# Performance work log

Hardware: AMD Instinct MI355X
Metric: run time of the kernel (lower is better)

## Reference

```python
import jax, jax.numpy as jnp
import numpy as np

HIDDEN = 2048
NUM_HEADS = 16
HEAD_DIM = HIDDEN // NUM_HEADS
WORLD_SIZE = 4
BATCH = 1
SEQ_SHARD = 2048


def setup_inputs() -> dict:
    key = jax.random.key(0)
    ks = jax.random.split(key, 9)
    s = 1.0 / np.sqrt(HIDDEN)
    return {
        'hidden_states': jax.random.normal(ks[0], (BATCH, SEQ_SHARD, HIDDEN), jnp.float32),
        'wq': jax.random.normal(ks[1], (HIDDEN, HIDDEN), jnp.float32) * s,
        'bq': jax.random.normal(ks[2], (HIDDEN,), jnp.float32) * s,
        'wk': jax.random.normal(ks[3], (HIDDEN, HIDDEN), jnp.float32) * s,
        'bk': jax.random.normal(ks[4], (HIDDEN,), jnp.float32) * s,
        'wv': jax.random.normal(ks[5], (HIDDEN, HIDDEN), jnp.float32) * s,
        'bv': jax.random.normal(ks[6], (HIDDEN,), jnp.float32) * s,
        'wo': jax.random.normal(ks[7], (HIDDEN, HIDDEN), jnp.float32) * s,
        'bo': jax.random.normal(ks[8], (HIDDEN,), jnp.float32) * s,
    }


def _ring_attention(q, k, v):
    # q, k, v: [B, H, S, D]. Simulation: every ring step receives the SAME
    # local KV shard (all_k_shards are clones of k), accumulated with
    # flash-style online softmax across WORLD_SIZE steps.
    B, H, S, D = q.shape
    scale = 1.0 / np.sqrt(D)
    output_acc = jnp.zeros_like(q)
    max_score = jnp.full((B, H, S, 1), -jnp.inf, dtype=q.dtype)
    sum_exp = jnp.zeros((B, H, S, 1), dtype=q.dtype)
    for _ in range(WORLD_SIZE):  # fixed small loop over ring steps
        scores = jnp.einsum('bhsd,bhtd->bhst', q, k) * scale  # [B,H,S,S]
        new_max = jnp.max(scores, axis=-1, keepdims=True)
        combined_max = jnp.maximum(max_score, new_max)
        old_scale = jnp.exp(max_score - combined_max)
        new_scale = jnp.exp(new_max - combined_max)
        new_exp = jnp.exp(scores - new_max)
        sum_exp = sum_exp * old_scale + jnp.sum(new_exp, axis=-1, keepdims=True) * new_scale
        output_acc = output_acc * old_scale + jnp.einsum('bhst,bhtd->bhsd', new_exp, v) * new_scale
        max_score = combined_max
    return output_acc / sum_exp


def reference(hidden_states, wq, bq, wk, bk, wv, bv, wo, bo):
    B, S, _ = hidden_states.shape
    # nn.Linear: y = x @ W^T + b
    q = hidden_states @ wq.T + bq
    k = hidden_states @ wk.T + bk
    v = hidden_states @ wv.T + bv
    split = lambda t: t.reshape(B, S, NUM_HEADS, HEAD_DIM).transpose(0, 2, 1, 3)
    attn = _ring_attention(split(q), split(k), split(v))  # [B,H,S,D]
    attn = attn.transpose(0, 2, 1, 3).reshape(B, S, HIDDEN)
    return attn @ wo.T + bo
```

## Files before the change

kernel.cpp:

```cpp
#include <hip/hip_runtime.h>
#include <hip/hip_bf16.h>
#include <stdint.h>

#define SEQ 2048
#define HID 2048
#define NH 16
#define HD 128
#define QSCALE_L2E 0.1275304429019769f

typedef __attribute__((ext_vector_type(4))) float f32x4;
typedef __attribute__((ext_vector_type(8))) short short8;
typedef __attribute__((ext_vector_type(4))) float f4;
typedef __attribute__((ext_vector_type(4))) unsigned short us4;

__device__ __forceinline__ unsigned short f2bu(float f) {
  union { float f; unsigned int u; } c; c.f = f;
  unsigned int u = c.u + 0x7fffu + ((c.u >> 16) & 1u);
  return (unsigned short)(u >> 16);
}

__device__ __forceinline__ unsigned short f2bu_fast(float f) {
  union { float f; unsigned int u; } c; c.f = f;
  return (unsigned short)((c.u + 0x8000u) >> 16);
}

__device__ __forceinline__ float b2f(unsigned short u) {
  union { unsigned int u; float f; } c; c.u = ((unsigned int)u) << 16; return c.f;
}

__device__ __forceinline__ float exp2fast(float x) {
  float r; asm("v_exp_f32 %0, %1" : "=v"(r) : "v"(x)); return r;
}

__device__ __forceinline__ void gload_lds16(const void* g, void* l) {
  __builtin_amdgcn_global_load_lds((const __attribute__((address_space(1))) void*)g,
                                   (__attribute__((address_space(3))) void*)l, 16, 0, 0);
}

#define BAR() __builtin_amdgcn_s_barrier()
#define LGKM0() do { asm volatile("s_waitcnt lgkmcnt(0)" ::: "memory"); __builtin_amdgcn_sched_barrier(0); } while (0)
#define VM6()   do { asm volatile("s_waitcnt vmcnt(6)"   ::: "memory"); __builtin_amdgcn_sched_barrier(0); } while (0)
#define VM4()   do { asm volatile("s_waitcnt vmcnt(4)"   ::: "memory"); __builtin_amdgcn_sched_barrier(0); } while (0)
#define VM0()   do { asm volatile("s_waitcnt vmcnt(0)"   ::: "memory"); __builtin_amdgcn_sched_barrier(0); } while (0)

__global__ __launch_bounds__(256) void cvt_kernel(
    const float* __restrict__ s0, const float* __restrict__ s1,
    const float* __restrict__ s2, const float* __restrict__ s3,
    const float* __restrict__ s4,
    unsigned short* __restrict__ d0, unsigned short* __restrict__ d1,
    unsigned short* __restrict__ d2, unsigned short* __restrict__ d3,
    unsigned short* __restrict__ d4, int n)
{
  const float* s; unsigned short* d;
  switch (blockIdx.y) {
    case 0: s = s0; d = d0; break;
    case 1: s = s1; d = d1; break;
    case 2: s = s2; d = d2; break;
    case 3: s = s3; d = d3; break;
    default: s = s4; d = d4; break;
  }
  const int stride = gridDim.x * blockDim.x;
  for (int i = blockIdx.x * blockDim.x + threadIdx.x; i * 8 < n; i += stride) {
    f4 v0 = *(const f4*)&s[i * 8];
    f4 v1 = *(const f4*)&s[i * 8 + 4];
    short8 o;
    o[0] = (short)f2bu(v0[0]); o[1] = (short)f2bu(v0[1]);
    o[2] = (short)f2bu(v0[2]); o[3] = (short)f2bu(v0[3]);
    o[4] = (short)f2bu(v1[0]); o[5] = (short)f2bu(v1[1]);
    o[6] = (short)f2bu(v1[2]); o[7] = (short)f2bu(v1[3]);
    *(short8*)&d[i * 8] = o;
  }
}

template<int MODE>
__global__ __launch_bounds__(256, 3) void gemm97(
    const unsigned short* __restrict__ A,
    const unsigned short* __restrict__ B,
    const float* __restrict__ b0, const float* __restrict__ b1, const float* __restrict__ b2,
    unsigned short* __restrict__ O0, unsigned short* __restrict__ O1, unsigned short* __restrict__ O2,
    float* __restrict__ Of, int M, int N, int K)
{
  extern __shared__ unsigned short lds[];
  const int tid = threadIdx.x;
  const int lane = tid & 63, w = tid >> 6;
  const int g = lane >> 4, q = lane & 15;
  const int wgM = w >> 1, wgN = w & 1;
  const long bm = (long)blockIdx.y * 128, bn = (long)blockIdx.x * 128;
  const int NK = K >> 6;

  const int srl = lane >> 3;
  const int scE = ((lane & 7) ^ srl) * 8;
  const int c0 = (g ^ (q & 7)) * 8;
  const int c1 = c0 ^ 32;
  const int aB = (wgM * 64 + q) * 64;
  const int bB = (wgN * 64 + q) * 64;

  f32x4 acc[4][4] = {};
  short8 a[4][2], b[4][2];

#define STAGE(gp, gbase, jj, ldsOff) do {                                     \
    _Pragma("unroll")                                                         \
    for (int c_ = 0; c_ < 4; ++c_) {                                          \
      const long row_ = (c_ * 4 + w) * 8 + srl;                               \
      gload_lds16(&(gp)[((gbase) + row_) * (long)K + (jj) * 64 + scE],        \
                  &lds[(ldsOff) + (c_ * 4 + w) * 512]);                       \
    }                                                                         \
  } while (0)

#define QUADD(n0, n1)                                                         \
  do {                                                                        \
    __builtin_amdgcn_s_setprio(1);                                            \
    _Pragma("unroll")                                                         \
    for (int mi_ = 0; mi_ < 4; ++mi_) {                                       \
      acc[mi_][n0] = __builtin_amdgcn_mfma_f32_16x16x32_bf16(                 \
          a[mi_][0], b[n0][0], acc[mi_][n0], 0, 0, 0);                        \
      acc[mi_][n0] = __builtin_amdgcn_mfma_f32_16x16x32_bf16(                 \
          a[mi_][1], b[n0][1], acc[mi_][n0], 0, 0, 0);                        \
      acc[mi_][n1] = __builtin_amdgcn_mfma_f32_16x16x32_bf16(                 \
          a[mi_][0], b[n1][0], acc[mi_][n1], 0, 0, 0);                        \
      acc[mi_][n1] = __builtin_amdgcn_mfma_f32_16x16x32_bf16(                 \
          a[mi_][1], b[n1][1], acc[mi_][n1], 0, 0, 0);                        \
    }                                                                         \
    __builtin_amdgcn_s_setprio(0);                                            \
  } while (0)

  for (int j = 0; j < NK; ++j) {
    STAGE(A, bm, j, 0);
    STAGE(B, bn, j, 8192);
    VM0();
    BAR();
#pragma unroll
    for (int mi = 0; mi < 4; ++mi) {
      a[mi][0] = *(const short8*)&lds[aB + mi * 1024 + c0];
      a[mi][1] = *(const short8*)&lds[aB + mi * 1024 + c1];
    }
#pragma unroll
    for (int ni = 0; ni < 4; ++ni) {
      b[ni][0] = *(const short8*)&lds[8192 + bB + ni * 1024 + c0];
      b[ni][1] = *(const short8*)&lds[8192 + bB + ni * 1024 + c1];
    }
    QUADD(0, 1);
    QUADD(2, 3);
    BAR();
  }

#pragma unroll
  for (int ni = 0; ni < 4; ++ni) {
    const int col = (int)bn + wgN * 64 + ni * 16 + q;
    float bv;
    if (MODE == 4) {
      const int which = col >> 11, c = col & 2047;
      const float* bp = which == 0 ? b0 : (which == 1 ? b1 : b2);
      bv = bp[c];
    } else {
      bv = b0[col];
    }
#pragma unroll
    for (int mi = 0; mi < 4; ++mi)
#pragma unroll
      for (int r = 0; r < 4; ++r) {
        const long row = bm + wgM * 64 + mi * 16 + 4 * g + r;
        const float v = acc[mi][ni][r] + bv;
        if (MODE == 4) {
          const int which = col >> 11, c = col & 2047, head = c >> 7, d = c & 127;
          if (which == 0)      O0[((long)head * SEQ + row) * HD + d] = f2bu(v * QSCALE_L2E);
          else if (which == 1) O1[((long)head * SEQ + row) * HD + d] = f2bu(v);
          else                 O2[((long)head * HD + d) * SEQ + row] = f2bu(v);
        } else {
          Of[row * (long)N + col] = v;
        }
      }
  }
#undef STAGE
#undef QUADD
}

template<int MODE>
__global__ __launch_bounds__(256, 2) void gemm128(
    const unsigned short* __restrict__ A,
    const unsigned short* __restrict__ B,
    const float* __restrict__ b0, const float* __restrict__ b1, const float* __restrict__ b2,
    unsigned short* __restrict__ O0, unsigned short* __restrict__ O1, unsigned short* __restrict__ O2,
    float* __restrict__ Of, int M, int N, int K)
{
  constexpr int ASZ = 64 * 64;
  constexpr int BSZ = 128 * 64;

  extern __shared__ unsigned short lds[];
  const int tid = threadIdx.x;
  const int lane = tid & 63, w = tid >> 6;
  const int g = lane >> 4, q = lane & 15;
  const long bm = (long)blockIdx.y * 64, bn = (long)blockIdx.x * 128;
  const int NK = K >> 6;

  const int srl = lane >> 3;
  const int scE = ((lane & 7) ^ srl) * 8;
  const int c0 = (g ^ (q & 7)) * 8;
  const int c1 = c0 ^ 32;
  const int aB = q * 64;
  const int bB = (w * 32 + q) * 64;

  f32x4 acc[4][2] = {};
  short8 a[4][2], b[2][2];

#define STAGE_A(jj) do {                                                      \
    unsigned short* dst_ = lds + (((jj) & 1) ? ASZ : 0);                      \
    _Pragma("unroll")                                                         \
    for (int c_ = 0; c_ < 2; ++c_) {                                          \
      const long row_ = (c_ * 4 + w) * 8 + srl;                               \
      gload_lds16(&A[(bm + row_) * (long)K + (jj) * 64 + scE],                \
                  &dst_[(c_ * 4 + w) * 512]);                                 \
    }                                                                         \
  } while (0)

#define STAGE_B(jj) do {                                                      \
    unsigned short* dst_ = lds + 2 * ASZ + (((jj) & 1) ? BSZ : 0);            \
    _Pragma("unroll")                                                         \
    for (int c_ = 0; c_ < 4; ++c_) {                                          \
      const long row_ = (c_ * 4 + w) * 8 + srl;                               \
      gload_lds16(&B[(bn + row_) * (long)K + (jj) * 64 + scE],                \
                  &dst_[(c_ * 4 + w) * 512]);                                 \
    }                                                                         \
  } while (0)

#define QUAD8(ni)                                                             \
  do {                                                                        \
    __builtin_amdgcn_s_setprio(1);                                            \
    _Pragma("unroll")                                                         \
    for (int mi_ = 0; mi_ < 4; ++mi_) {                                       \
      acc[mi_][ni] = __builtin_amdgcn_mfma_f32_16x16x32_bf16(                 \
          a[mi_][0], b[ni][0], acc[mi_][ni], 0, 0, 0);                        \
      acc[mi_][ni] = __builtin_amdgcn_mfma_f32_16x16x32_bf16(                 \
          a[mi_][1], b[ni][1], acc[mi_][ni], 0, 0, 0);                        \
    }                                                                         \
    __builtin_amdgcn_s_setprio(0);                                            \
  } while (0)

  STAGE_A(0); STAGE_B(0);
  STAGE_A(1); STAGE_B(1);
  VM6();
  BAR();

  for (int j = 0; j < NK; ++j) {
    unsigned short* At = lds + ((j & 1) ? ASZ : 0);
    unsigned short* Bt = lds + 2 * ASZ + ((j & 1) ? BSZ : 0);

#pragma unroll
    for (int mi = 0; mi < 4; ++mi) {
      a[mi][0] = *(const short8*)&At[aB + mi * 1024 + c0];
      a[mi][1] = *(const short8*)&At[aB + mi * 1024 + c1];
    }
#pragma unroll
    for (int ni = 0; ni < 2; ++ni) {
      b[ni][0] = *(const short8*)&Bt[bB + ni * 1024 + c0];
      b[ni][1] = *(const short8*)&Bt[bB + ni * 1024 + c1];
    }
    QUAD8(0);
    LGKM0();
    BAR();
    if (j + 2 < NK) { STAGE_A(j + 2); STAGE_B(j + 2); }
    QUAD8(1);
    if (j < NK - 2) { VM6(); } else { VM0(); }
    BAR();
  }

#pragma unroll
  for (int ni = 0; ni < 2; ++ni) {
    const int col = (int)bn + w * 32 + ni * 16 + q;
    float bv;
    if (MODE == 4) {
      const int which = col >> 11, c = col & 2047;
      const float* bp = which == 0 ? b0 : (which == 1 ? b1 : b2);
      bv = bp[c];
    } else {
      bv = b0[col];
    }
#pragma unroll
    for (int mi = 0; mi < 4; ++mi)
#pragma unroll
      for (int r = 0; r < 4; ++r) {
        const long row = bm + mi * 16 + 4 * g + r;
        const float v = acc[mi][ni][r] + bv;
        if (MODE == 4) {
          const int which = col >> 11, c = col & 2047, head = c >> 7, d = c & 127;
          if (which == 0)      O0[((long)head * SEQ + row) * HD + d] = f2bu(v * QSCALE_L2E);
          else if (which == 1) O1[((long)head * SEQ + row) * HD + d] = f2bu(v);
          else                 O2[((long)head * HD + d) * SEQ + row] = f2bu(v);
        } else {
          Of[row * (long)N + col] = v;
        }
      }
  }
#undef STAGE_A
#undef STAGE_B
#undef QUAD8
}

#define KVB 64
__global__ __launch_bounds__(256) void flash_attn(
    const unsigned short* __restrict__ Qb,
    const unsigned short* __restrict__ Kb,
    const unsigned short* __restrict__ VTb,
    unsigned short* __restrict__ attnb)
{
  extern __shared__ unsigned short S[];
  const int tid = threadIdx.x;
  const int l = tid & 63, w = tid >> 6;
  const int g = l >> 4, q = l & 15;
  const int bid = blockIdx.x;
  const int jj = bid >> 3;
  const int h = ((bid & 7) << 1) | (jj >> 5);
  const int qb = jj & 31;
  const int qrow0 = qb * 64 + w * 16;

  unsigned short* Pw = S + 32768 + w * 1024;

  short8 qf[4];
#pragma unroll
  for (int dc = 0; dc < 4; ++dc)
    qf[dc] = *(const short8*)&Qb[((long)h * SEQ + qrow0 + q) * HD + dc * 32 + g * 8];

  f32x4 oacc[8] = {};
  f32x4 saccA[4], saccB[4];
  const f32x4 zero4 = {};
  float lsum[4] = {0.f, 0.f, 0.f, 0.f};

  const unsigned short* Kg = Kb + (long)h * SEQ * HD;
  const unsigned short* Vg = VTb + (long)h * HD * SEQ;

  const int kce = ((l & 15) ^ (l >> 4)) * 8;
  const int kco = kce ^ 32;
  const int vce = ((l & 7) ^ ((l >> 3) & 7)) * 8;
  const int krl = l >> 4;
  const int vrl = l >> 3;
  unsigned short* KdB = S + w * 2048;
  unsigned short* VdB = S + 16384 + w * 2048;

#define STAGE_K(kb_, bufsel) do {                                             \
    const unsigned short* Kp_ = Kg + (long)((kb_) + w * 16 + krl) * HD;       \
    unsigned short* Kd_ = KdB + (bufsel) * 8192;                              \
    gload_lds16(Kp_ + 0 * 4 * HD + kce, Kd_ + 0 * 512);                       \
    gload_lds16(Kp_ + 1 * 4 * HD + kco, Kd_ + 1 * 512);                       \
    gload_lds16(Kp_ + 2 * 4 * HD + kce, Kd_ + 2 * 512);                       \
    gload_lds16(Kp_ + 3 * 4 * HD + kco, Kd_ + 3 * 512);                       \
  } while (0)

#define STAGE_V(kb_, bufsel) do {                                             \
    const unsigned short* Vp_ = Vg + (long)(w * 32 + vrl) * SEQ + (kb_) + vce;\
    unsigned short* Vd_ = VdB + (bufsel) * 8192;                              \
    gload_lds16(Vp_ + 0 * 8 * SEQ, Vd_ + 0 * 512);                            \
    gload_lds16(Vp_ + 1 * 8 * SEQ, Vd_ + 1 * 512);                            \
    gload_lds16(Vp_ + 2 * 8 * SEQ, Vd_ + 2 * 512);                            \
    gload_lds16(Vp_ + 3 * 8 * SEQ, Vd_ + 3 * 512);                            \
  } while (0)

#define QKT(T1, SN) do {                                                      \
    const unsigned short* Kt_ = S + ((T1) & 1) * 8192;                        \
    __builtin_amdgcn_s_setprio(1);                                            \
    _Pragma("unroll")                                                         \
    for (int kc = 0; kc < 4; ++kc) {                                          \
      const int krow_ = kc * 16 + q;                                          \
      const int sw_ = (krow_ & 7) << 4;                                       \
      _Pragma("unroll")                                                       \
      for (int dc = 0; dc < 4; ++dc) {                                        \
        short8 kf_ = *(const short8*)&Kt_[((krow_ * 256 + dc * 64 + g * 16) ^ sw_) >> 1]; \
        SN[kc] = __builtin_amdgcn_mfma_f32_16x16x32_bf16(qf[dc], kf_, SN[kc], 0, 0, 0);   \
      }                                                                       \
    }                                                                         \
    __builtin_amdgcn_s_setprio(0);                                            \
  } while (0)

#define FINISH_PV(T, SC) do {                                                 \
    float p_[4][4];                                                           \
    _Pragma("unroll")                                                         \
    for (int r = 0; r < 4; ++r) {                                             \
      _Pragma("unroll")                                                       \
      for (int kc = 0; kc < 4; ++kc) p_[kc][r] = exp2fast(SC[kc][r]);         \
      lsum[r] += (p_[0][r] + p_[1][r]) + (p_[2][r] + p_[3][r]);               \
    }                                                                         \
    _Pragma("unroll")                                                         \
    for (int r = 0; r < 4; ++r) {                                             \
      const int prow_ = 4 * g + r;                                            \
      const int sw_ = (prow_ & 7) << 4;                                       \
      _Pragma("unroll")                                                       \
      for (int kc = 0; kc < 4; ++kc)                                          \
        Pw[((prow_ * 128 + (kc * 16 + q) * 2) ^ sw_) >> 1] = f2bu_fast(p_[kc][r]); \
    }                                                                         \
    short8 pf_[2];                                                            \
    const int psw_ = (q & 7) << 4;                                            \
    _Pragma("unroll")                                                         \
    for (int ks = 0; ks < 2; ++ks)                                            \
      pf_[ks] = *(const short8*)&Pw[((q * 128 + ks * 64 + g * 16) ^ psw_) >> 1]; \
    const unsigned short* Vt_ = S + 16384 + ((T) & 1) * 8192;                 \
    __builtin_amdgcn_s_setprio(1);                                            \
    _Pragma("unroll")                                                         \
    for (int dt = 0; dt < 8; ++dt) {                                          \
      const int vrow_ = dt * 16 + q;                                          \
      _Pragma("unroll")                                                       \
      for (int ks = 0; ks < 2; ++ks) {                                        \
        short8 vf_ = *(const short8*)&Vt_[((vrow_ * 128 + ks * 64 + g * 16) ^ psw_) >> 1]; \
        oacc[dt] = __builtin_amdgcn_mfma_f32_16x16x32_bf16(pf_[ks], vf_, oacc[dt], 0, 0, 0); \
      }                                                                       \
    }                                                                         \
    __builtin_amdgcn_s_setprio(0);                                            \
  } while (0)

#define PHASE(T, SC, SN) do {                                                 \
    if ((T) + 2 < 32) STAGE_K(((T) + 2) * KVB, (T) & 1);                      \
    if ((T) + 1 < 32) {                                                       \
      _Pragma("unroll")                                                       \
      for (int kc = 0; kc < 4; ++kc) SN[kc] = zero4;                          \
      QKT((T) + 1, SN);                                                       \
    }                                                                         \
    FINISH_PV(T, SC);                                                         \
    BAR();                                                                    \
    if ((T) + 2 < 32) STAGE_V(((T) + 2) * KVB, (T) & 1);                      \
    if ((T) <= 29) { VM4(); } else { VM0(); }                                 \
    BAR();                                                                    \
  } while (0)

  STAGE_K(0, 0); STAGE_V(0, 0);
  STAGE_K(KVB, 1); STAGE_V(KVB, 1);
  VM0();
  BAR();
#pragma unroll
  for (int kc = 0; kc < 4; ++kc) saccA[kc] = zero4;
  QKT(0, saccA);
  BAR();

  for (int t = 0; t < 32; t += 2) {
    PHASE(t, saccA, saccB);
    PHASE(t + 1, saccB, saccA);
  }

#pragma unroll
  for (int off = 1; off < 16; off <<= 1)
#pragma unroll
    for (int r = 0; r < 4; ++r) lsum[r] += __shfl_xor(lsum[r], off);

  const float rl0 = 1.f / lsum[0], rl1 = 1.f / lsum[1];
  const float rl2 = 1.f / lsum[2], rl3 = 1.f / lsum[3];
#pragma unroll
  for (int dt = 0; dt < 8; ++dt) {
    const long colb = (long)h * HD + dt * 16 + q;
    attnb[(long)(qrow0 + 4 * g + 0) * HID + colb] = f2bu(oacc[dt][0] * rl0);
    attnb[(long)(qrow0 + 4 * g + 1) * HID + colb] = f2bu(oacc[dt][1] * rl1);
    attnb[(long)(qrow0 + 4 * g + 2) * HID + colb] = f2bu(oacc[dt][2] * rl2);
    attnb[(long)(qrow0 + 4 * g + 3) * HID + colb] = f2bu(oacc[dt][3] * rl3);
  }
#undef STAGE_K
#undef STAGE_V
#undef QKT
#undef FINISH_PV
#undef PHASE
}

extern "C" void kernel_launch(void* const* d_in, const int* in_sizes, int n_in,
                              void* d_out, int out_size, void* d_ws, size_t ws_size,
                              hipStream_t stream)
{
  const float* x  = (const float*)d_in[0];
  const float* wq = (const float*)d_in[1];
  const float* bq = (const float*)d_in[2];
  const float* wk = (const float*)d_in[3];
  const float* bk = (const float*)d_in[4];
  const float* wv = (const float*)d_in[5];
  const float* bv = (const float*)d_in[6];
  const float* wo = (const float*)d_in[7];
  const float* bo = (const float*)d_in[8];

  const long NEL = (long)HID * HID;
  unsigned short* Xb   = (unsigned short*)d_ws;
  unsigned short* Wqkv = Xb + NEL;
  unsigned short* Wob  = Wqkv + 3 * NEL;
  unsigned short* Qbuf = Wob + NEL;
  unsigned short* Kbuf = Qbuf + NEL;
  unsigned short* VTb  = Kbuf + NEL;
  unsigned short* Attn = VTb + NEL;

  static bool attrDone = false;
  if (!attrDone) {
    hipFuncSetAttribute(reinterpret_cast<const void*>(flash_attn),
                        hipFuncAttributeMaxDynamicSharedMemorySize, 73728);
    attrDone = true;
  }

  cvt_kernel<<<dim3(512, 5), 256, 0, stream>>>(
      x, wq, wk, wv, wo, Xb, Wqkv, Wqkv + NEL, Wqkv + 2 * NEL, Wob, (int)NEL);

  gemm97<4><<<dim3(48, 16), 256, 32768, stream>>>(
      Xb, Wqkv, bq, bk, bv, Qbuf, Kbuf, VTb, nullptr, SEQ, 3 * HID, HID);

  flash_attn<<<dim3(512), 256, 73728, stream>>>(Qbuf, Kbuf, VTb, Attn);

  gemm128<3><<<dim3(16, 32), 256, 49152, stream>>>(
      Attn, Wob, bo, nullptr, nullptr, nullptr, nullptr, nullptr,
      (float*)d_out, SEQ, HID, HID);
}
```

Before: 161.7 us.

## Repartition flash attention warps across KV columns and head-dim slices instead of query rows

Each wave now holds Q fragments for all 64 query rows and computes scores for its own 16-key slice. The probability tile is shared through LDS by all waves, and each wave accumulates the PV product for its own 32-column slice of the head dimension. Row sums are combined across waves through LDS at the end. The aim is to cut per-wave K and V LDS reads and register pressure from the 8 output accumulators. The cost is an extra barrier per tile, a shared P buffer, and more Q registers.

```diff
diff --git a/kernel.cpp b/kernel.cpp
--- a/kernel.cpp
+++ b/kernel.cpp
@@ -310,20 +310,22 @@
   const int bid = blockIdx.x;
   const int jj = bid >> 3;
   const int h = ((bid & 7) << 1) | (jj >> 5);
-  const int qb = jj & 31;
-  const int qrow0 = qb * 64 + w * 16;
-
-  unsigned short* Pw = S + 32768 + w * 1024;
-
-  short8 qf[4];
-#pragma unroll
-  for (int dc = 0; dc < 4; ++dc)
-    qf[dc] = *(const short8*)&Qb[((long)h * SEQ + qrow0 + q) * HD + dc * 32 + g * 8];
-
-  f32x4 oacc[8] = {};
+  const int qbk = jj & 31;
+  const long qbase = (long)qbk * 64;
+
+  unsigned short* Pt = S + 32768;
+
+  short8 qf[4][4];
+#pragma unroll
+  for (int qk = 0; qk < 4; ++qk)
+#pragma unroll
+    for (int dc = 0; dc < 4; ++dc)
+      qf[qk][dc] = *(const short8*)&Qb[((long)h * SEQ + qbase + qk * 16 + q) * HD + dc * 32 + g * 8];
+
+  f32x4 oacc[4][2] = {};
   f32x4 saccA[4], saccB[4];
   const f32x4 zero4 = {};
-  float lsum[4] = {0.f, 0.f, 0.f, 0.f};
+  float plsum[4][4] = {};
 
   const unsigned short* Kg = Kb + (long)h * SEQ * HD;
   const unsigned short* Vg = VTb + (long)h * HD * SEQ;
@@ -356,50 +358,51 @@
 
 #define QKT(T1, SN) do {                                                      \
     const unsigned short* Kt_ = S + ((T1) & 1) * 8192;                        \
+    const int krow_ = w * 16 + q;                                             \
+    const int ksw_ = (q & 7) << 4;                                            \
     __builtin_amdgcn_s_setprio(1);                                            \
     _Pragma("unroll")                                                         \
-    for (int kc = 0; kc < 4; ++kc) {                                          \
-      const int krow_ = kc * 16 + q;                                          \
-      const int sw_ = (krow_ & 7) << 4;                                       \
+    for (int dc = 0; dc < 4; ++dc) {                                          \
+      short8 kf_ = *(const short8*)&Kt_[((krow_ * 256 + dc * 64 + g * 16) ^ ksw_) >> 1]; \
       _Pragma("unroll")                                                       \
-      for (int dc = 0; dc < 4; ++dc) {                                        \
-        short8 kf_ = *(const short8*)&Kt_[((krow_ * 256 + dc * 64 + g * 16) ^ sw_) >> 1]; \
-        SN[kc] = __builtin_amdgcn_mfma_f32_16x16x32_bf16(qf[dc], kf_, SN[kc], 0, 0, 0);   \
+      for (int qk = 0; qk < 4; ++qk)                                          \
+        SN[qk] = __builtin_amdgcn_mfma_f32_16x16x32_bf16(qf[qk][dc], kf_, SN[qk], 0, 0, 0); \
+    }                                                                         \
+    __builtin_amdgcn_s_setprio(0);                                            \
+  } while (0)
+
+#define SOFT(SC) do {                                                         \
+    _Pragma("unroll")                                                         \
+    for (int qk = 0; qk < 4; ++qk)                                            \
+      _Pragma("unroll")                                                       \
+      for (int r = 0; r < 4; ++r) {                                           \
+        const float p_ = exp2fast(SC[qk][r]);                                 \
+        plsum[qk][r] += p_;                                                   \
+        const int qrow_ = qk * 16 + 4 * g + r;                                \
+        Pt[((qrow_ * 128 + (w * 16 + q) * 2) ^ ((qrow_ & 7) << 4)) >> 1] = f2bu_fast(p_); \
       }                                                                       \
-    }                                                                         \
-    __builtin_amdgcn_s_setprio(0);                                            \
-  } while (0)
-
-#define FINISH_PV(T, SC) do {                                                 \
-    float p_[4][4];                                                           \
-    _Pragma("unroll")                                                         \
-    for (int r = 0; r < 4; ++r) {                                             \
+  } while (0)
+
+#define PVPART(T) do {                                                        \
+    const unsigned short* Vt_ = S + 16384 + ((T) & 1) * 8192;                 \
+    const int psw_ = (q & 7) << 4;                                            \
+    short8 vfv_[2][2];                                                        \
+    _Pragma("unroll")                                                         \
+    for (int dtl = 0; dtl < 2; ++dtl) {                                       \
+      const int vrow_ = (2 * w + dtl) * 16 + q;                               \
+      vfv_[dtl][0] = *(const short8*)&Vt_[((vrow_ * 128 + 0 * 64 + g * 16) ^ psw_) >> 1]; \
+      vfv_[dtl][1] = *(const short8*)&Vt_[((vrow_ * 128 + 1 * 64 + g * 16) ^ psw_) >> 1]; \
+    }                                                                         \
+    __builtin_amdgcn_s_setprio(1);                                            \
+    _Pragma("unroll")                                                         \
+    for (int qk = 0; qk < 4; ++qk) {                                          \
+      const int prow_ = qk * 16 + q;                                          \
+      short8 pf0_ = *(const short8*)&Pt[((prow_ * 128 + 0 * 64 + g * 16) ^ psw_) >> 1]; \
+      short8 pf1_ = *(const short8*)&Pt[((prow_ * 128 + 1 * 64 + g * 16) ^ psw_) >> 1]; \
       _Pragma("unroll")                                                       \
-      for (int kc = 0; kc < 4; ++kc) p_[kc][r] = exp2fast(SC[kc][r]);         \
-      lsum[r] += (p_[0][r] + p_[1][r]) + (p_[2][r] + p_[3][r]);               \
-    }                                                                         \
-    _Pragma("unroll")                                                         \
-    for (int r = 0; r < 4; ++r) {                                             \
-      const int prow_ = 4 * g + r;                                            \
-      const int sw_ = (prow_ & 7) << 4;                                       \
-      _Pragma("unroll")                                                       \
-      for (int kc = 0; kc < 4; ++kc)                                          \
-        Pw[((prow_ * 128 + (kc * 16 + q) * 2) ^ sw_) >> 1] = f2bu_fast(p_[kc][r]); \
-    }                                                                         \
-    short8 pf_[2];                                                            \
-    const int psw_ = (q & 7) << 4;                                            \
-    _Pragma("unroll")                                                         \
-    for (int ks = 0; ks < 2; ++ks)                                            \
-      pf_[ks] = *(const short8*)&Pw[((q * 128 + ks * 64 + g * 16) ^ psw_) >> 1]; \
-    const unsigned short* Vt_ = S + 16384 + ((T) & 1) * 8192;                 \
-    __builtin_amdgcn_s_setprio(1);                                            \
-    _Pragma("unroll")                                                         \
-    for (int dt = 0; dt < 8; ++dt) {                                          \
-      const int vrow_ = dt * 16 + q;                                          \
-      _Pragma("unroll")                                                       \
-      for (int ks = 0; ks < 2; ++ks) {                                        \
-        short8 vf_ = *(const short8*)&Vt_[((vrow_ * 128 + ks * 64 + g * 16) ^ psw_) >> 1]; \
-        oacc[dt] = __builtin_amdgcn_mfma_f32_16x16x32_bf16(pf_[ks], vf_, oacc[dt], 0, 0, 0); \
+      for (int dtl = 0; dtl < 2; ++dtl) {                                     \
+        oacc[qk][dtl] = __builtin_amdgcn_mfma_f32_16x16x32_bf16(pf0_, vfv_[dtl][0], oacc[qk][dtl], 0, 0, 0); \
+        oacc[qk][dtl] = __builtin_amdgcn_mfma_f32_16x16x32_bf16(pf1_, vfv_[dtl][1], oacc[qk][dtl], 0, 0, 0); \
       }                                                                       \
     }                                                                         \
     __builtin_amdgcn_s_setprio(0);                                            \
@@ -409,14 +412,17 @@
     if ((T) + 2 < 32) STAGE_K(((T) + 2) * KVB, (T) & 1);                      \
     if ((T) + 1 < 32) {                                                       \
       _Pragma("unroll")                                                       \
-      for (int kc = 0; kc < 4; ++kc) SN[kc] = zero4;                          \
+      for (int qk_ = 0; qk_ < 4; ++qk_) SN[qk_] = zero4;                      \
       QKT((T) + 1, SN);                                                       \
     }                                                                         \
-    FINISH_PV(T, SC);                                                         \
-    BAR();                                                                    \
+    SOFT(SC);                                                                 \
+    LGKM0();                                                                  \
+    BAR();                                       \
+    PVPART(T);                                                                \
+    BAR();                                       \
     if ((T) + 2 < 32) STAGE_V(((T) + 2) * KVB, (T) & 1);                      \
     if ((T) <= 29) { VM4(); } else { VM0(); }                                 \
-    BAR();                                                                    \
+    BAR();                                       \
   } while (0)
 
   STAGE_K(0, 0); STAGE_V(0, 0);
@@ -424,7 +430,7 @@
   VM0();
   BAR();
 #pragma unroll
-  for (int kc = 0; kc < 4; ++kc) saccA[kc] = zero4;
+  for (int qk = 0; qk < 4; ++qk) saccA[qk] = zero4;
   QKT(0, saccA);
   BAR();
 
@@ -434,24 +440,40 @@
   }
 
 #pragma unroll
-  for (int off = 1; off < 16; off <<= 1)
-#pragma unroll
-    for (int r = 0; r < 4; ++r) lsum[r] += __shfl_xor(lsum[r], off);
-
-  const float rl0 = 1.f / lsum[0], rl1 = 1.f / lsum[1];
-  const float rl2 = 1.f / lsum[2], rl3 = 1.f / lsum[3];
-#pragma unroll
-  for (int dt = 0; dt < 8; ++dt) {
-    const long colb = (long)h * HD + dt * 16 + q;
-    attnb[(long)(qrow0 + 4 * g + 0) * HID + colb] = f2bu(oacc[dt][0] * rl0);
-    attnb[(long)(qrow0 + 4 * g + 1) * HID + colb] = f2bu(oacc[dt][1] * rl1);
-    attnb[(long)(qrow0 + 4 * g + 2) * HID + colb] = f2bu(oacc[dt][2] * rl2);
-    attnb[(long)(qrow0 + 4 * g + 3) * HID + colb] = f2bu(oacc[dt][3] * rl3);
-  }
+  for (int qk = 0; qk < 4; ++qk)
+#pragma unroll
+    for (int r = 0; r < 4; ++r)
+#pragma unroll
+      for (int off = 1; off < 16; off <<= 1)
+        plsum[qk][r] += __shfl_xor(plsum[qk][r], off);
+
+  __syncthreads();
+  float* Ls2 = (float*)(S + 32768);
+  if (q == 0) {
+#pragma unroll
+    for (int qk = 0; qk < 4; ++qk)
+#pragma unroll
+      for (int r = 0; r < 4; ++r)
+        Ls2[(qk * 16 + 4 * g + r) * 4 + w] = plsum[qk][r];
+  }
+  __syncthreads();
+
+#pragma unroll
+  for (int qk = 0; qk < 4; ++qk)
+#pragma unroll
+    for (int r = 0; r < 4; ++r) {
+      const int qrow = qk * 16 + 4 * g + r;
+      f4 lv = *(const f4*)&Ls2[qrow * 4];
+      const float rl = 1.f / ((lv[0] + lv[1]) + (lv[2] + lv[3]));
+      const long gbase = (qbase + qrow) * (long)HID + (long)h * HD;
+      attnb[gbase + (2 * w + 0) * 16 + q] = f2bu(oacc[qk][0][r] * rl);
+      attnb[gbase + (2 * w + 1) * 16 + q] = f2bu(oacc[qk][1][r] * rl);
+    }
 #undef STAGE_K
 #undef STAGE_V
 #undef QKT
-#undef FINISH_PV
+#undef SOFT
+#undef PVPART
 #undef PHASE
 }
 
```

After: 182.7 us. 13.0% more time.

## Replace double-buffered output GEMM with single-buffered kernel at higher occupancy

Applied to the files above, without the earlier changes.

The output projection GEMM drops its two-stage LDS double buffer and now loads each K tile, waits for it, then computes, using half the shared memory (24 KB instead of 48 KB). Launch bounds are raised to 3 blocks per CU so more workgroups can be resident and hide latency through occupancy rather than software pipelining. The unused MODE template path is also removed. In exchange, global loads no longer overlap with MFMA work inside a block, so each K step now carries full load latency plus two barriers.

```diff
diff --git a/kernel.cpp b/kernel.cpp
--- a/kernel.cpp
+++ b/kernel.cpp
@@ -175,17 +175,12 @@
 #undef QUADD
 }
 
-template<int MODE>
-__global__ __launch_bounds__(256, 2) void gemm128(
+__global__ __launch_bounds__(256, 3) void gemm97o(
     const unsigned short* __restrict__ A,
     const unsigned short* __restrict__ B,
-    const float* __restrict__ b0, const float* __restrict__ b1, const float* __restrict__ b2,
-    unsigned short* __restrict__ O0, unsigned short* __restrict__ O1, unsigned short* __restrict__ O2,
+    const float* __restrict__ b0,
     float* __restrict__ Of, int M, int N, int K)
 {
-  constexpr int ASZ = 64 * 64;
-  constexpr int BSZ = 128 * 64;
-
   extern __shared__ unsigned short lds[];
   const int tid = threadIdx.x;
   const int lane = tid & 63, w = tid >> 6;
@@ -204,22 +199,20 @@
   short8 a[4][2], b[2][2];
 
 #define STAGE_A(jj) do {                                                      \
-    unsigned short* dst_ = lds + (((jj) & 1) ? ASZ : 0);                      \
     _Pragma("unroll")                                                         \
     for (int c_ = 0; c_ < 2; ++c_) {                                          \
       const long row_ = (c_ * 4 + w) * 8 + srl;                               \
       gload_lds16(&A[(bm + row_) * (long)K + (jj) * 64 + scE],                \
-                  &dst_[(c_ * 4 + w) * 512]);                                 \
+                  &lds[(c_ * 4 + w) * 512]);                                  \
     }                                                                         \
   } while (0)
 
 #define STAGE_B(jj) do {                                                      \
-    unsigned short* dst_ = lds + 2 * ASZ + (((jj) & 1) ? BSZ : 0);            \
     _Pragma("unroll")                                                         \
     for (int c_ = 0; c_ < 4; ++c_) {                                          \
       const long row_ = (c_ * 4 + w) * 8 + srl;                               \
       gload_lds16(&B[(bn + row_) * (long)K + (jj) * 64 + scE],                \
-                  &dst_[(c_ * 4 + w) * 512]);                                 \
+                  &lds[4096 + (c_ * 4 + w) * 512]);                           \
     }                                                                         \
   } while (0)
 
@@ -236,59 +229,36 @@
     __builtin_amdgcn_s_setprio(0);                                            \
   } while (0)
 
-  STAGE_A(0); STAGE_B(0);
-  STAGE_A(1); STAGE_B(1);
-  VM6();
-  BAR();
-
   for (int j = 0; j < NK; ++j) {
-    unsigned short* At = lds + ((j & 1) ? ASZ : 0);
-    unsigned short* Bt = lds + 2 * ASZ + ((j & 1) ? BSZ : 0);
-
+    STAGE_A(j);
+    STAGE_B(j);
+    VM0();
+    BAR();
 #pragma unroll
     for (int mi = 0; mi < 4; ++mi) {
-      a[mi][0] = *(const short8*)&At[aB + mi * 1024 + c0];
-      a[mi][1] = *(const short8*)&At[aB + mi * 1024 + c1];
+      a[mi][0] = *(const short8*)&lds[aB + mi * 1024 + c0];
+      a[mi][1] = *(const short8*)&lds[aB + mi * 1024 + c1];
     }
 #pragma unroll
     for (int ni = 0; ni < 2; ++ni) {
-      b[ni][0] = *(const short8*)&Bt[bB + ni * 1024 + c0];
-      b[ni][1] = *(const short8*)&Bt[bB + ni * 1024 + c1];
+      b[ni][0] = *(const short8*)&lds[4096 + bB + ni * 1024 + c0];
+      b[ni][1] = *(const short8*)&lds[4096 + bB + ni * 1024 + c1];
     }
     QUAD8(0);
-    LGKM0();
-    BAR();
-    if (j + 2 < NK) { STAGE_A(j + 2); STAGE_B(j + 2); }
     QUAD8(1);
-    if (j < NK - 2) { VM6(); } else { VM0(); }
     BAR();
   }
 
 #pragma unroll
   for (int ni = 0; ni < 2; ++ni) {
     const int col = (int)bn + w * 32 + ni * 16 + q;
-    float bv;
-    if (MODE == 4) {
-      const int which = col >> 11, c = col & 2047;
-      const float* bp = which == 0 ? b0 : (which == 1 ? b1 : b2);
-      bv = bp[c];
-    } else {
-      bv = b0[col];
-    }
+    const float bv = b0[col];
 #pragma unroll
     for (int mi = 0; mi < 4; ++mi)
 #pragma unroll
       for (int r = 0; r < 4; ++r) {
         const long row = bm + mi * 16 + 4 * g + r;
-        const float v = acc[mi][ni][r] + bv;
-        if (MODE == 4) {
-          const int which = col >> 11, c = col & 2047, head = c >> 7, d = c & 127;
-          if (which == 0)      O0[((long)head * SEQ + row) * HD + d] = f2bu(v * QSCALE_L2E);
-          else if (which == 1) O1[((long)head * SEQ + row) * HD + d] = f2bu(v);
-          else                 O2[((long)head * HD + d) * SEQ + row] = f2bu(v);
-        } else {
-          Of[row * (long)N + col] = v;
-        }
+        Of[row * (long)N + col] = acc[mi][ni][r] + bv;
       }
   }
 #undef STAGE_A
@@ -493,7 +463,6 @@
 
   flash_attn<<<dim3(512), 256, 73728, stream>>>(Qbuf, Kbuf, VTb, Attn);
 
-  gemm128<3><<<dim3(16, 32), 256, 49152, stream>>>(
-      Attn, Wob, bo, nullptr, nullptr, nullptr, nullptr, nullptr,
-      (float*)d_out, SEQ, HID, HID);
-}
+  gemm97o<<<dim3(16, 32), 256, 24576, stream>>>(
+      Attn, Wob, bo, (float*)d_out, SEQ, HID, HID);
+}
```

Result: slower. 169.0 us (+4.5%).
